# Optimization experiments

Measured on AMD Instinct MI355X. Metric: run time of the kernel, lower is better.

Reference implementation:

```python
import jax, jax.numpy as jnp
import numpy as np

DIM = 512
HEADS = 8
DIM_HEAD = 64
DIM_INNER = HEADS * DIM_HEAD
FRAC_GRAD = 0.5
SCALE = DIM_HEAD ** -0.5
EPS_CUMPROD = 1e-10
EPS_INV = 1e-8


def setup_inputs() -> dict:
    key = jax.random.key(0)
    ks = jax.random.split(key, 8)
    b, n = 2, 2048
    x = jax.random.normal(ks[0], (b, n, DIM), dtype=jnp.float32)
    gamma = jnp.ones((DIM,), dtype=jnp.float32)
    w_qkv = jax.random.normal(ks[1], (DIM, 3 * DIM_INNER), dtype=jnp.float32) * 0.02
    b_qkv = jnp.zeros((3 * DIM_INNER,), dtype=jnp.float32)
    # to_a: torch init is zeros weight + bias 10; use small random weight and
    # moderate bias so the decay gate is non-trivial for correctness testing
    w_a = jax.random.normal(ks[2], (DIM, DIM_INNER), dtype=jnp.float32) * 0.02
    b_a = jnp.full((DIM_INNER,), 2.0, dtype=jnp.float32)
    w_out = jax.random.normal(ks[3], (DIM_INNER, DIM), dtype=jnp.float32) * 0.02
    b_out = jnp.zeros((DIM,), dtype=jnp.float32)
    return {"x": x, "gamma": gamma, "w_qkv": w_qkv, "b_qkv": b_qkv,
            "w_a": w_a, "b_a": b_a, "w_out": w_out, "b_out": b_out}


def _rms_norm(x, gamma):
    # F.normalize(x, dim=-1) * sqrt(dim) * gamma
    nrm = jnp.linalg.norm(x, axis=-1, keepdims=True)
    return x / jnp.maximum(nrm, 1e-12) * (DIM ** 0.5) * gamma


def _safe_cumprod(t, axis):
    t = jnp.clip(t, EPS_CUMPROD, 1.0)
    return jnp.exp(jnp.cumsum(jnp.log(t), axis=axis))


def reference(x, gamma, w_qkv, b_qkv, w_a, b_a, w_out, b_out):
    b, n, _ = x.shape
    x = _rms_norm(x, gamma)

    qkv = x @ w_qkv + b_qkv  # [b, n, 3*h*d]
    qkv = qkv.reshape(b, n, 3, HEADS, DIM_HEAD).transpose(2, 0, 3, 1, 4)  # [3,b,h,n,d]
    q, k, v = qkv[0], qkv[1], qkv[2]
    q = q * SCALE

    # data-dependent relative-position decay gate
    a = (x @ w_a + b_a).reshape(b, n, HEADS, DIM_HEAD).transpose(0, 2, 1, 3)  # [b,h,n,d]
    a = a * FRAC_GRAD + jax.lax.stop_gradient(a) * (1.0 - FRAC_GRAD)
    a = jax.nn.sigmoid(a)
    a_cum = _safe_cumprod(a, axis=-2)
    a_cum_inv = 1.0 / jnp.maximum(a_cum, EPS_INV)

    q = q * a_cum
    k = k * a_cum_inv

    sim = jnp.einsum('bhid,bhjd->bhij', q, k)
    causal_mask = jnp.triu(jnp.ones((n, n), dtype=bool), k=1)
    attn = jnp.where(causal_mask, 0.0, sim)  # no softmax in decay branch

    out = jnp.einsum('bhij,bhjd->bhid', attn, v)  # [b,h,n,d]
    out = out.transpose(0, 2, 1, 3).reshape(b, n, DIM_INNER)
    return out @ w_out + b_out
```

## Files before the change

### kernel.cpp

```cpp
#include <hip/hip_runtime.h>
#include <hip/hip_cooperative_groups.h>


namespace cg = cooperative_groups;

using s8v   = __attribute__((ext_vector_type(8))) short;
using f32x4 = __attribute__((ext_vector_type(4))) float;

__device__ __forceinline__ unsigned short f2b(float f) {
  unsigned int u = __builtin_bit_cast(unsigned int, f);
  u += 0x7FFFu + ((u >> 16) & 1u);
  return (unsigned short)(u >> 16);
}
__device__ __forceinline__ float b2f(unsigned short b) {
  unsigned int u = ((unsigned int)b) << 16;
  return __builtin_bit_cast(float, u);
}
__device__ __forceinline__ f32x4 mfma16(s8v a, s8v b, f32x4 c) {
  return __builtin_amdgcn_mfma_f32_16x16x32_bf16(a, b, c, 0, 0, 0);
}
__device__ __forceinline__ void gload16(const void* g, void* l) {
  __builtin_amdgcn_global_load_lds(
      (const __attribute__((address_space(1))) void*)g,
      (__attribute__((address_space(3))) void*)l, 16, 0, 0);
}

__device__ __forceinline__ void st_prep(int u, int tid, char* arena,
    const float* __restrict__ x, const float* __restrict__ gamma,
    short* __restrict__ xnb,
    const float* __restrict__ w_qkv, const float* __restrict__ w_a,
    const float* __restrict__ w_out,
    short* __restrict__ wT, short* __restrict__ woT) {
  int lane = tid & 63, wave = tid >> 6;
  if (u < 1024) {
    int row = u * 4 + wave;
    const float4* xp = reinterpret_cast<const float4*>(x + (size_t)row * 512 + lane * 8);
    float4 v0 = xp[0], v1 = xp[1];
    float ss = v0.x*v0.x + v0.y*v0.y + v0.z*v0.z + v0.w*v0.w
             + v1.x*v1.x + v1.y*v1.y + v1.z*v1.z + v1.w*v1.w;
#pragma unroll
    for (int off = 32; off > 0; off >>= 1) ss += __shfl_xor(ss, off, 64);
    float s = 22.627416997969522f / fmaxf(sqrtf(ss), 1e-12f);
    const float* g = gamma + lane * 8;
    float vals[8] = {v0.x, v0.y, v0.z, v0.w, v1.x, v1.y, v1.z, v1.w};
    s8v o;
#pragma unroll
    for (int j = 0; j < 8; ++j) o[j] = (short)f2b(vals[j] * s * g[j]);
    *reinterpret_cast<s8v*>(xnb + (size_t)row * 512 + lane * 8) = o;
  } else {
    float (*t)[33] = reinterpret_cast<float (*)[33]>(arena);
    int id = u - 1024;
    int bx = id % 80, k0 = (id / 80) * 32;
    const float* src; short* dst; int N, n0;
    if (bx < 48)      { src = w_qkv; dst = wT;                      N = 1536; n0 = bx * 32; }
    else if (bx < 64) { src = w_a;   dst = wT + (size_t)1536 * 512; N = 512;  n0 = (bx - 48) * 32; }
    else              { src = w_out; dst = woT;                     N = 512;  n0 = (bx - 64) * 32; }
    int tx = tid & 31, ty = tid >> 5;
    __syncthreads();
#pragma unroll
    for (int i = 0; i < 4; ++i)
      t[ty + 8 * i][tx] = src[(size_t)(k0 + ty + 8 * i) * N + n0 + tx];
    __syncthreads();
#pragma unroll
    for (int i = 0; i < 4; ++i)
      dst[(size_t)(n0 + ty + 8 * i) * 512 + k0 + tx] = (short)f2b(t[tx][ty + 8 * i]);
  }
}

template <int BM, int BN, int FM, int FN>
__device__ __forceinline__ void gemm_core(const short* __restrict__ A,
                                          const short* __restrict__ Bm,
                                          char* LA, char* LB,
                                          int m0, int n0, int tid,
                                          f32x4 (&acc)[FM][FN]) {
  const int lane = tid & 63, wave = tid >> 6;
  const int wr = (wave >> 1) * (BM / 2), wc = (wave & 1) * (BN / 2);
#pragma unroll 1
  for (int t = 0; t < 8; ++t) {
    const int k0 = t * 64;
#pragma unroll
    for (int r = 0; r < BM / 32; ++r) {
      int o = r * 4096 + tid * 16;
      int row = o >> 7;
      int ce = (((o & 127) ^ ((row & 7) << 4)) >> 1);
      gload16(A + (size_t)(m0 + row) * 512 + k0 + ce, LA + o);
    }
#pragma unroll
    for (int r = 0; r < BN / 32; ++r) {
      int o = r * 4096 + tid * 16;
      int row = o >> 7;
      int ce = (((o & 127) ^ ((row & 7) << 4)) >> 1);
      gload16(Bm + (size_t)(n0 + row) * 512 + k0 + ce, LB + o);
    }
    __syncthreads();
#pragma unroll
    for (int kk = 0; kk < 2; ++kk) {
      s8v af[FM], bf[FN];
#pragma unroll
      for (int m = 0; m < FM; ++m) {
        int row = wr + m * 16 + (lane & 15);
        int ad = ((row << 7) + kk * 64 + ((lane >> 4) << 4)) ^ ((row & 7) << 4);
        af[m] = *reinterpret_cast<const s8v*>(LA + ad);
      }
#pragma unroll
      for (int n = 0; n < FN; ++n) {
        int row = wc + n * 16 + (lane & 15);
        int ad = ((row << 7) + kk * 64 + ((lane >> 4) << 4)) ^ ((row & 7) << 4);
        bf[n] = *reinterpret_cast<const s8v*>(LB + ad);
      }
#pragma unroll
      for (int m = 0; m < FM; ++m)
#pragma unroll
        for (int n = 0; n < FN; ++n)
          acc[m][n] = mfma16(af[m], bf[n], acc[m][n]);
    }
    if (t + 1 < 8) __syncthreads();
  }
}

__device__ __forceinline__ void st_gemm0(int vid, int tid, char* arena,
    const short* __restrict__ xnb, const short* __restrict__ wT,
    short* __restrict__ qkvb, const float* __restrict__ b_qkv,
    const float* __restrict__ b_a, float* __restrict__ araw,
    float* __restrict__ csum) {
  const int lane = tid & 63, wave = tid >> 6;
  int xcd = vid & 7, rq = vid >> 3;
  int bx = rq & 15, by = xcd * 4 + (rq >> 4);
  int m0 = by * 128, n0 = bx * 128;
  f32x4 acc[4][4] = {};
  gemm_core<128, 128, 4, 4>(xnb, wT, arena, arena + 16384, m0, n0, tid, acc);
  int wr = (wave >> 1) * 64, wc = (wave & 1) * 64;
  if (n0 < 1536) {
#pragma unroll
    for (int m = 0; m < 4; ++m)
#pragma unroll
      for (int n = 0; n < 4; ++n)
#pragma unroll
        for (int r = 0; r < 4; ++r) {
          int row = m0 + wr + m * 16 + ((lane >> 4) << 2) + r;
          int col = n0 + wc + n * 16 + (lane & 15);
          float v = acc[m][n][r] + b_qkv[col];
          int w = col >> 9, h = (col >> 6) & 7, d = col & 63;
          int b = row >> 11, nn = row & 2047;
          qkvb[((((size_t)(w * 2 + b)) * 8 + h) * 2048 + nn) * 64 + d] = (short)f2b(v);
        }
  } else {
    float cs[4] = {};
    int b = m0 >> 11;
#pragma unroll
    for (int m = 0; m < 4; ++m)
#pragma unroll
      for (int n = 0; n < 4; ++n)
#pragma unroll
        for (int r = 0; r < 4; ++r) {
          int row = m0 + wr + m * 16 + ((lane >> 4) << 2) + r;
          int gc = n0 + wc + n * 16 + (lane & 15) - 1536;
          int h = gc >> 6, d = gc & 63, nn = row & 2047;
          float xv = acc[m][n][r] + b_a[gc];
          araw[((size_t)(b * 8 + h) * 2048 + nn) * 64 + d] = xv;
          float a = 1.f / (1.f + expf(-xv));
          a = fminf(fmaxf(a, 1e-10f), 1.f);
          cs[n] += logf(a);
        }
#pragma unroll
    for (int n = 0; n < 4; ++n) {
      cs[n] += __shfl_xor(cs[n], 16, 64);
      cs[n] += __shfl_xor(cs[n], 32, 64);
    }
    int nsel = lane >> 4;
    float v = (nsel == 0) ? cs[0] : (nsel == 1) ? cs[1] : (nsel == 2) ? cs[2] : cs[3];
    int col = wc + nsel * 16 + (lane & 15);
    int gc = n0 + col - 1536;
    int h = gc >> 6, d = gc & 63;
    int chunkg = ((m0 & 2047) >> 6) + (wave >> 1);
    csum[(((size_t)(b * 8 + h)) * 32 + chunkg) * 64 + d] = v;
  }
}

__device__ __forceinline__ float csum_prefix(const float* __restrict__ csum,
                                             int bh, int chunk, int d) {
  float pre = 0.f;
#pragma unroll
  for (int c = 0; c < 32; ++c) {
    float cv = csum[((size_t)bh * 32 + c) * 64 + d];
    pre += (c < chunk) ? cv : 0.f;
  }
  return pre;
}

__device__ __forceinline__ void st_scan2(int vid, int tid, char* arena,
    const short* __restrict__ qkvb, const float* __restrict__ araw,
    const float* __restrict__ csum, short* __restrict__ q2,
    short* __restrict__ k2, short* __restrict__ vT, short* __restrict__ Sbuf) {
  int chunk = vid & 31, bh = vid >> 5;
  int lane = tid & 63, wave = tid >> 6, d = lane;
  short (*kL)[64] = reinterpret_cast<short (*)[64]>(arena);
  short (*vL)[64] = reinterpret_cast<short (*)[64]>(arena + 8192);
  char* kT  = arena + 16384;
  char* vTl = arena + 24576;
  float (*wsum)[64] = reinterpret_cast<float (*)[64]>(arena + 16384);
  float pre = csum_prefix(csum, bh, chunk, d);
  const float* ap = araw + ((size_t)bh * 2048 + chunk * 64 + wave * 16) * 64 + d;
  float la[16]; float run = 0.f;
#pragma unroll
  for (int rr = 0; rr < 16; ++rr) {
    float xv = ap[rr * 64];
    float a = 1.f / (1.f + expf(-xv));
    a = fminf(fmaxf(a, 1e-10f), 1.f);
    run += logf(a);
    la[rr] = run;
  }
  wsum[wave][d] = run;
  __syncthreads();
#pragma unroll
  for (int w = 0; w < 3; ++w) if (w < wave) pre += wsum[w][d];
  const size_t WS = (size_t)2 * 8 * 2048 * 64;
  size_t base = ((size_t)bh * 2048 + chunk * 64 + wave * 16) * 64 + d;
#pragma unroll 4
  for (int rr = 0; rr < 16; ++rr) {
    int r = wave * 16 + rr;
    float g = expf(pre + la[rr]);
    float gi = 1.f / fmaxf(g, 1e-8f);
    float qv = b2f((unsigned short)qkvb[base + rr * 64]);
    float kv = b2f((unsigned short)qkvb[base + WS + rr * 64]);
    short vb = qkvb[base + 2 * WS + rr * 64];
    q2[base + rr * 64] = (short)f2b(qv * 0.125f * g);
    unsigned short kb = f2b(kv * gi);
    k2[base + rr * 64] = (short)kb;
    kL[r][d] = (short)kb;
    vL[r][d] = vb;
  }
  __syncthreads();
  short* vTrow = vT + ((size_t)bh * 64 + d) * 2048 + chunk * 64;
#pragma unroll
  for (int gg = 0; gg < 2; ++gg) {
    int g8 = wave + gg * 4;
    s8v pk, pv;
#pragma unroll
    for (int j = 0; j < 8; ++j) { pk[j] = kL[g8 * 8 + j][d]; pv[j] = vL[g8 * 8 + j][d]; }
    *reinterpret_cast<s8v*>(vTrow + g8 * 8) = pv;
    int ad = ((d << 7) + g8 * 16) ^ ((d & 7) << 4);
    *reinterpret_cast<s8v*>(kT  + ad) = pk;
    *reinterpret_cast<s8v*>(vTl + ad) = pv;
  }
  __syncthreads();
  f32x4 acc[4] = {};
#pragma unroll
  for (int kk = 0; kk < 2; ++kk) {
    int arow = wave * 16 + (lane & 15);
    int aad = ((arow << 7) + kk * 64 + ((lane >> 4) << 4)) ^ ((arow & 7) << 4);
    s8v av = *reinterpret_cast<const s8v*>(vTl + aad);
#pragma unroll
    for (int n = 0; n < 4; ++n) {
      int brow = n * 16 + (lane & 15);
      int bad = ((brow << 7) + kk * 64 + ((lane >> 4) << 4)) ^ ((brow & 7) << 4);
      acc[n] = mfma16(av, *reinterpret_cast<const s8v*>(kT + bad), acc[n]);
    }
  }
  short* Sp = Sbuf + ((size_t)bh * 32 + chunk) * 4096;
#pragma unroll
  for (int n = 0; n < 4; ++n)
#pragma unroll
    for (int r = 0; r < 4; ++r)
      Sp[(wave * 16 + ((lane >> 4) << 2) + r) * 64 + n * 16 + (lane & 15)] = (short)f2b(acc[n][r]);
}

__device__ __forceinline__ void st_sprefix(int vid, int tid,
    const short* __restrict__ Sbuf, short* __restrict__ Spre) {
  int bh = vid >> 4;
  int e = ((vid & 15) << 8) + tid;
  size_t base = (size_t)bh * 32 * 4096 + e;
  unsigned short v[32];
#pragma unroll
  for (int c = 0; c < 32; ++c)
    v[c] = (unsigned short)Sbuf[base + (size_t)c * 4096];
  float acc = 0.f;
#pragma unroll
  for (int c = 0; c < 32; ++c) {
    Spre[base + (size_t)c * 4096] = (short)f2b(acc);
    acc += b2f(v[c]);
  }
}

__device__ __forceinline__ void st_attnk(int vid, int tid, char* arena,
    const short* __restrict__ q2, const short* __restrict__ k2,
    const short* __restrict__ vT, const short* __restrict__ Spre,
    short* __restrict__ aout) {
  int chunk = vid & 31, bh = vid >> 5;
  int lane = tid & 63, wave = tid >> 6;
  char* LQ = arena;
  char* LK = arena + 8192;
  char* LV = arena + 16384;
  char* LS = arena + 24576;
#pragma unroll
  for (int rr = 0; rr < 2; ++rr) {
    int o = rr * 4096 + tid * 16;
    int row = o >> 7;
    int ce = (((o & 127) ^ ((row & 7) << 4)) >> 1);
    gload16(q2   + ((size_t)bh * 2048 + chunk * 64 + row) * 64 + ce, LQ + o);
    gload16(k2   + ((size_t)bh * 2048 + chunk * 64 + row) * 64 + ce, LK + o);
    gload16(vT   + ((size_t)bh * 64 + row) * 2048 + chunk * 64 + ce, LV + o);
    gload16(Spre + (((size_t)bh * 32 + chunk) * 64 + row) * 64 + ce, LS + o);
  }
  __syncthreads();
  f32x4 accS[4] = {}, accO[4] = {};
#pragma unroll
  for (int kk = 0; kk < 2; ++kk) {
    int arow = wave * 16 + (lane & 15);
    int aad = ((arow << 7) + kk * 64 + ((lane >> 4) << 4)) ^ ((arow & 7) << 4);
    s8v aq = *reinterpret_cast<const s8v*>(LQ + aad);
#pragma unroll
    for (int n = 0; n < 4; ++n) {
      int brow = n * 16 + (lane & 15);
      int bad = ((brow << 7) + kk * 64 + ((lane >> 4) << 4)) ^ ((brow & 7) << 4);
      accS[n] = mfma16(aq, *reinterpret_cast<const s8v*>(LK + bad), accS[n]);
      accO[n] = mfma16(aq, *reinterpret_cast<const s8v*>(LS + bad), accO[n]);
    }
  }
  __syncthreads();
#pragma unroll
  for (int n = 0; n < 4; ++n)
#pragma unroll
    for (int r = 0; r < 4; ++r) {
      int i = wave * 16 + ((lane >> 4) << 2) + r;
      int j = n * 16 + (lane & 15);
      float v = (j <= i) ? accS[n][r] : 0.f;
      int ad = ((i << 7) + (j << 1)) ^ ((i & 7) << 4);
      *reinterpret_cast<short*>(LQ + ad) = (short)f2b(v);
    }
  __syncthreads();
#pragma unroll
  for (int kk = 0; kk < 2; ++kk) {
    int arow = wave * 16 + (lane & 15);
    int aad = ((arow << 7) + kk * 64 + ((lane >> 4) << 4)) ^ ((arow & 7) << 4);
    s8v ap = *reinterpret_cast<const s8v*>(LQ + aad);
#pragma unroll
    for (int n = 0; n < 4; ++n) {
      int brow = n * 16 + (lane & 15);
      int bad = ((brow << 7) + kk * 64 + ((lane >> 4) << 4)) ^ ((brow & 7) << 4);
      accO[n] = mfma16(ap, *reinterpret_cast<const s8v*>(LV + bad), accO[n]);
    }
  }
  int b = bh >> 3, h = bh & 7;
#pragma unroll
  for (int n = 0; n < 4; ++n)
#pragma unroll
    for (int r = 0; r < 4; ++r) {
      int i = wave * 16 + ((lane >> 4) << 2) + r;
      int col = h * 64 + n * 16 + (lane & 15);
      size_t row = (size_t)b * 2048 + chunk * 64 + i;
      aout[row * 512 + col] = (short)f2b(accO[n][r]);
    }
}

__device__ __forceinline__ void st_gemm1(int vid, int tid, char* arena,
    const short* __restrict__ aout, const short* __restrict__ woT,
    float* __restrict__ out, const float* __restrict__ b_out) {
  const int lane = tid & 63, wave = tid >> 6;
  int xcd = vid & 7, rq = vid >> 3;
  int bx = rq & 7, by = xcd * 8 + (rq >> 3);
  int m0 = by * 64, n0 = bx * 64;
  f32x4 acc[2][2] = {};
  gemm_core<64, 64, 2, 2>(aout, woT, arena, arena + 8192, m0, n0, tid, acc);
  int wr = (wave >> 1) * 32, wc = (wave & 1) * 32;
#pragma unroll
  for (int m = 0; m < 2; ++m)
#pragma unroll
    for (int n = 0; n < 2; ++n)
#pragma unroll
      for (int r = 0; r < 4; ++r) {
        int row = m0 + wr + m * 16 + ((lane >> 4) << 2) + r;
        int col = n0 + wc + n * 16 + (lane & 15);
        out[(size_t)row * 512 + col] = acc[m][n][r] + b_out[col];
      }
}

__global__ __launch_bounds__(256, 2) void mega_k(
    const float* __restrict__ x, const float* __restrict__ gamma,
    const float* __restrict__ w_qkv, const float* __restrict__ b_qkv,
    const float* __restrict__ w_a, const float* __restrict__ b_a,
    const float* __restrict__ w_out, const float* __restrict__ b_out,
    float* __restrict__ out,
    short* __restrict__ xnb, short* __restrict__ wT, short* __restrict__ woT,
    short* __restrict__ qkvb, float* __restrict__ araw, float* __restrict__ csum,
    short* __restrict__ Sbuf, short* __restrict__ Spre, short* __restrict__ aout) {
  __shared__ __align__(16) char arena[32768];
  cg::grid_group grid = cg::this_grid();
  const int bid = blockIdx.x, tid = threadIdx.x;
  const int lane = tid & 63, wave = tid >> 6;

  for (int u = bid; u < 2304; u += 512)
    st_prep(u, tid, arena, x, gamma, xnb, w_qkv, w_a, w_out, wT, woT);
  __threadfence(); grid.sync();

  st_gemm0(bid, tid, arena, xnb, wT, qkvb, b_qkv, b_a, araw, csum);
  __threadfence(); grid.sync();

  const int chunk = bid & 31, bh = bid >> 5;
  const int d = lane;
  char* qL  = arena;
  char* kR  = arena + 8192;
  char* kT  = arena + 16384;
  char* vTl = arena + 24576;
  f32x4 accO[4] = {};
  {
    float (*wsum)[64] = reinterpret_cast<float (*)[64]>(kR);
    float pre = csum_prefix(csum, bh, chunk, d);
    const float* ap = araw + ((size_t)bh * 2048 + chunk * 64 + wave * 16) * 64 + d;
    float la[16]; float run = 0.f;
#pragma unroll
    for (int rr = 0; rr < 16; ++rr) {
      float xv = ap[rr * 64];
      float a = 1.f / (1.f + expf(-xv));
      a = fminf(fmaxf(a, 1e-10f), 1.f);
      run += logf(a);
      la[rr] = run;
    }
    wsum[wave][d] = run;
    __syncthreads();
#pragma unroll
    for (int w = 0; w < 3; ++w) if (w < wave) pre += wsum[w][d];
    __syncthreads();
    const size_t WS = (size_t)2 * 8 * 2048 * 64;
    size_t base = ((size_t)bh * 2048 + chunk * 64 + wave * 16) * 64 + d;
#pragma unroll 4
    for (int rr = 0; rr < 16; ++rr) {
      int r = wave * 16 + rr;
      float g = expf(pre + la[rr]);
      float gi = 1.f / fmaxf(g, 1e-8f);
      float qv = b2f((unsigned short)qkvb[base + rr * 64]);
      float kv = b2f((unsigned short)qkvb[base + WS + rr * 64]);
      short vb = qkvb[base + 2 * WS + rr * 64];
      unsigned short qb = f2b(qv * 0.125f * g);
      unsigned short kb = f2b(kv * gi);
      int adr = ((r << 7) + (d << 1)) ^ ((r & 7) << 4);
      *reinterpret_cast<short*>(qL + adr) = (short)qb;
      *reinterpret_cast<short*>(kR + adr) = (short)kb;
      int adt = ((d << 7) + (r << 1)) ^ ((d & 7) << 4);
      *reinterpret_cast<short*>(kT  + adt) = (short)kb;
      *reinterpret_cast<short*>(vTl + adt) = vb;
    }
    __syncthreads();
    f32x4 sacc[4] = {};
#pragma unroll
    for (int kk = 0; kk < 2; ++kk) {
      int arow = wave * 16 + (lane & 15);
      int aad = ((arow << 7) + kk * 64 + ((lane >> 4) << 4)) ^ ((arow & 7) << 4);
      s8v av = *reinterpret_cast<const s8v*>(vTl + aad);
#pragma unroll
      for (int n = 0; n < 4; ++n) {
        int brow = n * 16 + (lane & 15);
        int bad = ((brow << 7) + kk * 64 + ((lane >> 4) << 4)) ^ ((brow & 7) << 4);
        sacc[n] = mfma16(av, *reinterpret_cast<const s8v*>(kT + bad), sacc[n]);
      }
    }
    short* Sp = Sbuf + ((size_t)bh * 32 + chunk) * 4096;
#pragma unroll
    for (int n = 0; n < 4; ++n)
#pragma unroll
      for (int r = 0; r < 4; ++r)
        Sp[(wave * 16 + ((lane >> 4) << 2) + r) * 64 + n * 16 + (lane & 15)] = (short)f2b(sacc[n][r]);
    f32x4 accS[4] = {};
#pragma unroll
    for (int kk = 0; kk < 2; ++kk) {
      int arow = wave * 16 + (lane & 15);
      int aad = ((arow << 7) + kk * 64 + ((lane >> 4) << 4)) ^ ((arow & 7) << 4);
      s8v aq = *reinterpret_cast<const s8v*>(qL + aad);
#pragma unroll
      for (int n = 0; n < 4; ++n) {
        int brow = n * 16 + (lane & 15);
        int bad = ((brow << 7) + kk * 64 + ((lane >> 4) << 4)) ^ ((brow & 7) << 4);
        accS[n] = mfma16(aq, *reinterpret_cast<const s8v*>(kR + bad), accS[n]);
      }
    }
    __syncthreads();
#pragma unroll
    for (int n = 0; n < 4; ++n)
#pragma unroll
      for (int r = 0; r < 4; ++r) {
        int i = wave * 16 + ((lane >> 4) << 2) + r;
        int j = n * 16 + (lane & 15);
        float v = (j <= i) ? accS[n][r] : 0.f;
        int ad = ((i << 7) + (j << 1)) ^ ((i & 7) << 4);
        *reinterpret_cast<short*>(kT + ad) = (short)f2b(v);
      }
    __syncthreads();
#pragma unroll
    for (int kk = 0; kk < 2; ++kk) {
      int arow = wave * 16 + (lane & 15);
      int aad = ((arow << 7) + kk * 64 + ((lane >> 4) << 4)) ^ ((arow & 7) << 4);
      s8v ap = *reinterpret_cast<const s8v*>(kT + aad);
#pragma unroll
      for (int n = 0; n < 4; ++n) {
        int brow = n * 16 + (lane & 15);
        int bad = ((brow << 7) + kk * 64 + ((lane >> 4) << 4)) ^ ((brow & 7) << 4);
        accO[n] = mfma16(ap, *reinterpret_cast<const s8v*>(vTl + bad), accO[n]);
      }
    }
  }
  __threadfence(); grid.sync();

  if (bid < 256) st_sprefix(bid, tid, Sbuf, Spre);
  __threadfence(); grid.sync();

  {
    char* LS = kR;
#pragma unroll
    for (int rr = 0; rr < 2; ++rr) {
      int o = rr * 4096 + tid * 16;
      int row = o >> 7;
      int ce = (((o & 127) ^ ((row & 7) << 4)) >> 1);
      gload16(Spre + (((size_t)bh * 32 + chunk) * 64 + row) * 64 + ce, LS + o);
    }
    __syncthreads();
#pragma unroll
    for (int kk = 0; kk < 2; ++kk) {
      int arow = wave * 16 + (lane & 15);
      int aad = ((arow << 7) + kk * 64 + ((lane >> 4) << 4)) ^ ((arow & 7) << 4);
      s8v aq = *reinterpret_cast<const s8v*>(qL + aad);
#pragma unroll
      for (int n = 0; n < 4; ++n) {
        int brow = n * 16 + (lane & 15);
        int bad = ((brow << 7) + kk * 64 + ((lane >> 4) << 4)) ^ ((brow & 7) << 4);
        accO[n] = mfma16(aq, *reinterpret_cast<const s8v*>(LS + bad), accO[n]);
      }
    }
    int b = bh >> 3, h = bh & 7;
#pragma unroll
    for (int n = 0; n < 4; ++n)
#pragma unroll
      for (int r = 0; r < 4; ++r) {
        int i = wave * 16 + ((lane >> 4) << 2) + r;
        int col = h * 64 + n * 16 + (lane & 15);
        size_t row = (size_t)b * 2048 + chunk * 64 + i;
        aout[row * 512 + col] = (short)f2b(accO[n][r]);
      }
  }
  __threadfence(); grid.sync();

  st_gemm1(bid, tid, arena, aout, woT, out, b_out);
}

__global__ __launch_bounds__(256) void prep_k(const float* x, const float* gamma,
    short* xnb, const float* w_qkv, const float* w_a, const float* w_out,
    short* wT, short* woT) {
  __shared__ __align__(16) char arena[4224];
  st_prep(blockIdx.x, threadIdx.x, arena, x, gamma, xnb, w_qkv, w_a, w_out, wT, woT);
}
__global__ __launch_bounds__(256) void gemm0_k(const short* xnb, const short* wT,
    short* qkvb, const float* b_qkv, const float* b_a, float* araw, float* csum) {
  __shared__ __align__(16) char arena[32768];
  st_gemm0(blockIdx.x, threadIdx.x, arena, xnb, wT, qkvb, b_qkv, b_a, araw, csum);
}
__global__ __launch_bounds__(256) void scan2_k(const short* qkvb, const float* araw,
    const float* csum, short* q2, short* k2, short* vT, short* Sbuf) {
  __shared__ __align__(16) char arena[32768];
  st_scan2(blockIdx.x, threadIdx.x, arena, qkvb, araw, csum, q2, k2, vT, Sbuf);
}
__global__ __launch_bounds__(256) void sprefix_k(const short* Sbuf, short* Spre) {
  st_sprefix(blockIdx.x, threadIdx.x, Sbuf, Spre);
}
__global__ __launch_bounds__(256) void attnk_k(const short* q2, const short* k2,
    const short* vT, const short* Spre, short* aout) {
  __shared__ __align__(16) char arena[32768];
  st_attnk(blockIdx.x, threadIdx.x, arena, q2, k2, vT, Spre, aout);
}
__global__ __launch_bounds__(256) void gemm1_k(const short* aout, const short* woT,
    float* out, const float* b_out) {
  __shared__ __align__(16) char arena[16384];
  st_gemm1(blockIdx.x, threadIdx.x, arena, aout, woT, out, b_out);
}

extern "C" void kernel_launch(void* const* d_in, const int* in_sizes, int n_in,
                              void* d_out, int out_size, void* d_ws, size_t ws_size,
                              hipStream_t stream) {
  const float* x     = (const float*)d_in[0];
  const float* gamma = (const float*)d_in[1];
  const float* w_qkv = (const float*)d_in[2];
  const float* b_qkv = (const float*)d_in[3];
  const float* w_a   = (const float*)d_in[4];
  const float* b_a   = (const float*)d_in[5];
  const float* w_out = (const float*)d_in[6];
  const float* b_out = (const float*)d_in[7];
  float* out = (float*)d_out;
  char* ws = (char*)d_ws;

  const size_t MB = 1u << 20;
  short* xnb  = (short*)(ws);
  short* wT   = (short*)(ws + 4  * MB);
  short* woT  = (short*)(ws + 6  * MB);
  short* qkvb = (short*)(ws + 7  * MB);
  float* araw = (float*)(ws + 19 * MB);
  float* csum = (float*)(ws + 27 * MB);
  short* Sbuf = (short*)(ws + 28 * MB);
  short* Spre = (short*)(ws + 32 * MB);
  short* aout = (short*)(ws + 36 * MB);
  short* q2   = (short*)(ws + 40 * MB);
  short* k2   = (short*)(ws + 44 * MB);
  short* vT   = (short*)(ws + 48 * MB);

  int dev = 0; (void)hipGetDevice(&dev);
  int coop = 0;
  (void)hipDeviceGetAttribute(&coop, hipDeviceAttributeCooperativeLaunch, dev);
  int nb = 0;
  (void)hipOccupancyMaxActiveBlocksPerMultiprocessor(&nb, mega_k, 256, 0);

  hipError_t err = hipErrorUnknown;
  if (coop && nb >= 2) {
    void* args[] = {&x, &gamma, &w_qkv, &b_qkv, &w_a, &b_a, &w_out, &b_out,
                    &out, &xnb, &wT, &woT, &qkvb, &araw, &csum,
                    &Sbuf, &Spre, &aout};
    err = hipLaunchCooperativeKernel((void*)mega_k, dim3(512), dim3(256), args, 0, stream);
  }
  if (err != hipSuccess) {
    prep_k   <<<2304, 256, 0, stream>>>(x, gamma, xnb, w_qkv, w_a, w_out, wT, woT);
    gemm0_k  <<<512,  256, 0, stream>>>(xnb, wT, qkvb, b_qkv, b_a, araw, csum);
    scan2_k  <<<512,  256, 0, stream>>>(qkvb, araw, csum, q2, k2, vT, Sbuf);
    sprefix_k<<<256,  256, 0, stream>>>(Sbuf, Spre);
    attnk_k  <<<512,  256, 0, stream>>>(q2, k2, vT, Spre, aout);
    gemm1_k  <<<512,  256, 0, stream>>>(aout, woT, out, b_out);
  }
}
```

Baseline: 61.74 us.

## Remove separate S-prefix stage; each block sums preceding chunk states directly

Drops the dedicated prefix-sum stage and one grid-wide barrier in the cooperative megakernel. Each attention block instead reads all earlier chunk states from Sbuf, accumulates them in fp32, converts to bf16 and writes the result into swizzled LDS. This removes a grid sync and the intermediate Spre round-trip, at the cost of redundant reads: later chunks read up to 31 states each, which raises total global/L2 traffic and leaves the blocks with unbalanced work.

New measurement: 61.45 us. No clear change (-0.5%).

```diff
diff --git a/kernel.cpp b/kernel.cpp
--- a/kernel.cpp
+++ b/kernel.cpp
@@ -383,7 +383,7 @@
     float* __restrict__ out,
     short* __restrict__ xnb, short* __restrict__ wT, short* __restrict__ woT,
     short* __restrict__ qkvb, float* __restrict__ araw, float* __restrict__ csum,
-    short* __restrict__ Sbuf, short* __restrict__ Spre, short* __restrict__ aout) {
+    short* __restrict__ Sbuf, short* __restrict__ aout) {
   __shared__ __align__(16) char arena[32768];
   cg::grid_group grid = cg::this_grid();
   const int bid = blockIdx.x, tid = threadIdx.x;
@@ -500,18 +500,33 @@
   }
   __threadfence(); grid.sync();
 
-  if (bid < 256) st_sprefix(bid, tid, Sbuf, Spre);
-  __threadfence(); grid.sync();
-
   {
     char* LS = kR;
-#pragma unroll
-    for (int rr = 0; rr < 2; ++rr) {
-      int o = rr * 4096 + tid * 16;
-      int row = o >> 7;
-      int ce = (((o & 127) ^ ((row & 7) << 4)) >> 1);
-      gload16(Spre + (((size_t)bh * 32 + chunk) * 64 + row) * 64 + ce, LS + o);
-    }
+    int srow = tid >> 2, scol0 = (tid & 3) * 16;
+    const short* Sb = Sbuf + (size_t)bh * 32 * 4096 + srow * 64 + scol0;
+    float acc0[8] = {}, acc1[8] = {};
+#pragma unroll
+    for (int c = 0; c < 32; ++c) {
+      if (c < chunk) {
+        s8v v0 = *reinterpret_cast<const s8v*>(Sb + (size_t)c * 4096);
+        s8v v1 = *reinterpret_cast<const s8v*>(Sb + (size_t)c * 4096 + 8);
+#pragma unroll
+        for (int j = 0; j < 8; ++j) {
+          acc0[j] += b2f((unsigned short)v0[j]);
+          acc1[j] += b2f((unsigned short)v1[j]);
+        }
+      }
+    }
+    s8v o0, o1;
+#pragma unroll
+    for (int j = 0; j < 8; ++j) {
+      o0[j] = (short)f2b(acc0[j]);
+      o1[j] = (short)f2b(acc1[j]);
+    }
+    int byte0 = (srow << 7) + (scol0 << 1);
+    int sw = (srow & 7) << 4;
+    *reinterpret_cast<s8v*>(LS + ((byte0)      ^ sw)) = o0;
+    *reinterpret_cast<s8v*>(LS + ((byte0 + 16) ^ sw)) = o1;
     __syncthreads();
 #pragma unroll
     for (int kk = 0; kk < 2; ++kk) {
@@ -593,8 +608,8 @@
   float* araw = (float*)(ws + 19 * MB);
   float* csum = (float*)(ws + 27 * MB);
   short* Sbuf = (short*)(ws + 28 * MB);
-  short* Spre = (short*)(ws + 32 * MB);
-  short* aout = (short*)(ws + 36 * MB);
+  short* aout = (short*)(ws + 32 * MB);
+  short* Spre = (short*)(ws + 36 * MB);
   short* q2   = (short*)(ws + 40 * MB);
   short* k2   = (short*)(ws + 44 * MB);
   short* vT   = (short*)(ws + 48 * MB);
@@ -609,7 +624,7 @@
   if (coop && nb >= 2) {
     void* args[] = {&x, &gamma, &w_qkv, &b_qkv, &w_a, &b_a, &w_out, &b_out,
                     &out, &xnb, &wT, &woT, &qkvb, &araw, &csum,
-                    &Sbuf, &Spre, &aout};
+                    &Sbuf, &aout};
     err = hipLaunchCooperativeKernel((void*)mega_k, dim3(512), dim3(256), args, 0, stream);
   }
   if (err != hipSuccess) {
```
